# Optimization experiments

Measured on AMD Instinct MI355X. Metric: run time of the kernel, lower is better.

## Reference

```python
import jax, jax.numpy as jnp
import numpy as np

N, E = 20000, 640000
S_DIM, V_DIM, E_DIM = 128, 32 // 2, 32
EPS = 1e-8


def _vector_norm(v):
    # v: [N, V, 3] -> [N, V]
    return jnp.sqrt(jnp.clip((v * v).sum(-1), EPS))


def _gvp(s, v, W1, b1, W2, b2, Wv, Wg, bg):
    """SimpleGVP: s [N,s_in], v [N,v_in,3] -> (s_out [N,s_out], v_out [N,v_out,3]).
    Weights stored [in, out] (transpose of torch Linear)."""
    vn = _vector_norm(v)                                   # [N, v_in]
    h = jnp.concatenate([s, vn], axis=-1) @ W1 + b1        # [N, s_out]
    s_out = jax.nn.silu(h) @ W2 + b2                       # [N, s_out]
    v_proj = jnp.einsum('nvc,vw->nwc', v, Wv)              # [N, v_out, 3]
    gate = jax.nn.sigmoid(s_out @ Wg + bg)[..., None]      # [N, v_out, 1]
    return s_out, v_proj * gate


def _layer_norm(x, g, b, eps=1e-5):
    mu = x.mean(-1, keepdims=True)
    var = ((x - mu) ** 2).mean(-1, keepdims=True)
    return (x - mu) * jax.lax.rsqrt(var + eps) * g + b


def _linear_params(key, fan_in, fan_out, bias=True):
    kw, kb = jax.random.split(key)
    lim = 1.0 / np.sqrt(fan_in)
    W = jax.random.uniform(kw, (fan_in, fan_out), jnp.float32, -lim, lim)
    if bias:
        b = jax.random.uniform(kb, (fan_out,), jnp.float32, -lim, lim)
        return W, b
    return (W,)


def setup_inputs() -> dict:
    key = jax.random.key(0)
    ks = jax.random.split(key, 16)
    s = jax.random.normal(ks[0], (N, S_DIM), jnp.float32)
    v = jax.random.normal(ks[1], (N, V_DIM, 3), jnp.float32)
    edge_index = jax.random.randint(ks[2], (2, E), 0, N, jnp.int32)
    edge_s = jax.random.normal(ks[3], (E, E_DIM), jnp.float32)
    edge_v = jax.random.normal(ks[4], (E, 1, 3), jnp.float32)

    # message GVP: s_in = 2*S + E_DIM + 1 (+v_in norms), v_in = 2*V + 1
    ms_in, mv_in = 2 * S_DIM + E_DIM + 1, 2 * V_DIM + 1
    msg_W1, msg_b1 = _linear_params(ks[5], ms_in + mv_in, S_DIM)
    msg_W2, msg_b2 = _linear_params(ks[6], S_DIM, S_DIM)
    (msg_Wv,) = _linear_params(ks[7], mv_in, V_DIM, bias=False)
    msg_Wg, msg_bg = _linear_params(ks[8], S_DIM, V_DIM)

    # update GVP: s_in = 2*S, v_in = 2*V
    us_in, uv_in = 2 * S_DIM, 2 * V_DIM
    upd_W1, upd_b1 = _linear_params(ks[9], us_in + uv_in, S_DIM)
    upd_W2, upd_b2 = _linear_params(ks[10], S_DIM, S_DIM)
    (upd_Wv,) = _linear_params(ks[11], uv_in, V_DIM, bias=False)
    upd_Wg, upd_bg = _linear_params(ks[12], S_DIM, V_DIM)

    ln_g = jnp.ones((S_DIM,), jnp.float32)
    ln_b = jnp.zeros((S_DIM,), jnp.float32)

    return dict(s=s, v=v, edge_index=edge_index, edge_s=edge_s, edge_v=edge_v,
                msg_W1=msg_W1, msg_b1=msg_b1, msg_W2=msg_W2, msg_b2=msg_b2,
                msg_Wv=msg_Wv, msg_Wg=msg_Wg, msg_bg=msg_bg,
                upd_W1=upd_W1, upd_b1=upd_b1, upd_W2=upd_W2, upd_b2=upd_b2,
                upd_Wv=upd_Wv, upd_Wg=upd_Wg, upd_bg=upd_bg,
                ln_g=ln_g, ln_b=ln_b)


def reference(s, v, edge_index, edge_s, edge_v,
              msg_W1, msg_b1, msg_W2, msg_b2, msg_Wv, msg_Wg, msg_bg,
              upd_W1, upd_b1, upd_W2, upd_b2, upd_Wv, upd_Wg, upd_bg,
              ln_g, ln_b):
    src, dst = edge_index[0], edge_index[1]
    n = s.shape[0]

    # 1) per-edge message inputs (gather)
    edge_len = _vector_norm(edge_v)                                   # [E, 1]
    m_s_in = jnp.concatenate([s[src], s[dst], edge_s, edge_len], -1)  # [E, 2S+e+1]
    m_v_in = jnp.concatenate([v[src], v[dst], edge_v], 1)             # [E, 2V+1, 3]
    m_s, m_v = _gvp(m_s_in, m_v_in, msg_W1, msg_b1, msg_W2, msg_b2,
                    msg_Wv, msg_Wg, msg_bg)

    # 2) scatter-add aggregation at destination nodes
    agg_s = jax.ops.segment_sum(m_s, dst, num_segments=n)             # [N, S]
    agg_v = jax.ops.segment_sum(m_v, dst, num_segments=n)             # [N, V, 3]

    # 3) residual update
    u_s_in = jnp.concatenate([s, agg_s], -1)
    u_v_in = jnp.concatenate([v, agg_v], 1)
    ds, dv = _gvp(u_s_in, u_v_in, upd_W1, upd_b1, upd_W2, upd_b2,
                  upd_Wv, upd_Wg, upd_bg)

    s_out = _layer_norm(s + ds, ln_g, ln_b)
    v_out = v + dv
    return s_out, v_out
```

## Files before the change

kernel.cpp:

```cpp
#include <hip/hip_runtime.h>

typedef __attribute__((ext_vector_type(4))) float floatx4;
typedef __attribute__((ext_vector_type(8))) short shortx8;
typedef __attribute__((ext_vector_type(4))) short shortx4;
typedef __attribute__((ext_vector_type(4))) int intx4;
typedef __attribute__((ext_vector_type(2))) int intx2;

#define DEVI static __device__ __forceinline__

constexpr int NN = 20000;
constexpr int NE = 640000;

constexpr size_t W1ET_OFF = 0;
constexpr size_t WLEN_OFF = 8192;
constexpr size_t WCAT_OFF = 8704;
constexpr size_t W2T_OFF  = 90624;
constexpr size_t WGT_OFF  = 123392;
constexpr size_t U1T_OFF  = 127488;
constexpr size_t U2T_OFF  = 201216;
constexpr size_t UGT_OFF  = 233984;
constexpr size_t ASRC_OFF = 238080;
constexpr size_t ADST_OFF = ASRC_OFF + (size_t)NN * 128 * 2;
constexpr size_t BSRC_OFF = ADST_OFF + (size_t)NN * 128 * 2;
constexpr size_t BDST_OFF = BSRC_OFF + (size_t)NN * 64 * 2;
constexpr size_t AGG_S_OFF = BDST_OFF + (size_t)NN * 64 * 2;
constexpr size_t AGG_V_OFF = AGG_S_OFF + (size_t)NN * 128 * 2;
constexpr size_t CNT_OFF  = AGG_V_OFF + (size_t)NN * 64 * 2;
constexpr size_t OFF_OFF  = CNT_OFF + (size_t)NN * 4;
constexpr size_t PERM_OFF = OFF_OFF + (size_t)NN * 4;
constexpr size_t SD_OFF   = PERM_OFF + (size_t)NE * 4;
constexpr size_t LEV_OFF  = SD_OFF + (size_t)NE * 8;
constexpr size_t MEMSET_BYTES = (size_t)NN * 128 * 2 + (size_t)NN * 64 * 2 + (size_t)NN * 4;

DEVI float bf2f(short h) {
  union { unsigned u; float f; } c;
  c.u = ((unsigned)(unsigned short)h) << 16;
  return c.f;
}
DEVI short f2bf(float f) {
  union { float f; unsigned u; } c; c.f = f;
  unsigned x = c.u;
  return (short)((x + 0x7fffu + ((x >> 16) & 1u)) >> 16);
}
DEVI int pack2bf(float x, float y) {
  return (int)(unsigned short)f2bf(x) | ((int)(unsigned short)f2bf(y) << 16);
}
DEVI void atom_pk(short* addr, int val) {
  asm volatile("global_atomic_pk_add_bf16 %0, %1, off" : : "v"(addr), "v"(val) : "memory");
}
DEVI float sigm(float x) { return 1.0f / (1.0f + __expf(-x)); }

DEVI floatx4 mfma16(shortx8 a, shortx8 b, floatx4 c) {
  return __builtin_amdgcn_mfma_f32_16x16x32_bf16(a, b, c, 0, 0, 0);
}

__global__ void gvp_prep(const float* __restrict__ mW1, const float* __restrict__ mW2,
                         const float* __restrict__ mWg, const float* __restrict__ uW1,
                         const float* __restrict__ uW2, const float* __restrict__ uWg,
                         short* __restrict__ w1et, float* __restrict__ wlen,
                         short* __restrict__ wcat, short* __restrict__ w2t,
                         short* __restrict__ wgt, short* __restrict__ u1t,
                         short* __restrict__ u2t, short* __restrict__ ugt) {
  int i = blockIdx.x * 256 + threadIdx.x;
  if (i < 4096) { int n = i >> 5, k = i & 31; w1et[i] = f2bf(mW1[(256 + k) * 128 + n]); return; }
  i -= 4096;
  if (i < 128) { wlen[i] = mW1[288 * 128 + i] + mW1[321 * 128 + i]; return; }
  i -= 128;
  if (i < 40960) {
    int n = i / 160, k = i % 160;
    float val = 0.f;
    if (n < 128) {
      if (k < 128) val = mW1[k * 128 + n];
      else if (k < 144) val = mW1[(161 + k) * 128 + n];
    } else {
      int n2 = n - 128;
      if (k < 128) val = mW1[(128 + k) * 128 + n2];
      else if (k < 144) val = mW1[(177 + k) * 128 + n2];
    }
    wcat[i] = f2bf(val);
    return;
  }
  i -= 40960;
  if (i < 16384) { int n = i >> 7, k = i & 127; w2t[i] = f2bf(mW2[k * 128 + n]); return; }
  i -= 16384;
  if (i < 2048) { int g = i >> 7, k = i & 127; wgt[i] = f2bf(mWg[k * 16 + g]); return; }
  i -= 2048;
  if (i < 36864) { int n = i / 288, k = i % 288; u1t[i] = f2bf(uW1[k * 128 + n]); return; }
  i -= 36864;
  if (i < 16384) { int n = i >> 7, k = i & 127; u2t[i] = f2bf(uW2[k * 128 + n]); return; }
  i -= 16384;
  if (i < 2048) { int g = i >> 7, k = i & 127; ugt[i] = f2bf(uWg[k * 16 + g]); return; }
}

__global__ void gvp_hist(const int* __restrict__ eidx, int* __restrict__ cnt) {
  int e = blockIdx.x * 256 + threadIdx.x;
  if (e < NE) atomicAdd(cnt + eidx[NE + e], 1);
}

__global__ void gvp_scan(const int* __restrict__ cnt, int* __restrict__ off) {
  __shared__ int part[256];
  const int t = threadIdx.x;
  const int base = t * 79;
  int sum = 0;
  for (int j = 0; j < 79; ++j) {
    int i = base + j;
    if (i < NN) sum += cnt[i];
  }
  part[t] = sum;
  __syncthreads();
  if (t == 0) {
    int run = 0;
    for (int i = 0; i < 256; ++i) { int c = part[i]; part[i] = run; run += c; }
  }
  __syncthreads();
  int run = part[t];
  for (int j = 0; j < 79; ++j) {
    int i = base + j;
    if (i < NN) { off[i] = run; run += cnt[i]; }
  }
}

__global__ void gvp_scatter(const int* __restrict__ eidx, const float* __restrict__ ev,
                            int* __restrict__ off, int* __restrict__ perm,
                            int* __restrict__ sd, float* __restrict__ lev) {
  int e = blockIdx.x * 256 + threadIdx.x;
  if (e >= NE) return;
  int sn = eidx[e], d = eidx[NE + e];
  int pos = atomicAdd(off + d, 1);
  perm[pos] = e;
  intx2 p; p[0] = sn; p[1] = d;
  *(intx2*)(sd + (size_t)pos * 2) = p;
  const float* evp = ev + (size_t)e * 3;
  float x = evp[0], y = evp[1], z = evp[2];
  floatx4 q;
  q[0] = x; q[1] = y; q[2] = z;
  q[3] = sqrtf(fmaxf(x * x + y * y + z * z, 1e-8f));
  *(floatx4*)(lev + (size_t)pos * 4) = q;
}

__global__ __launch_bounds__(256) void gvp_nodepre(
    const float* __restrict__ s, const float* __restrict__ v,
    const short* __restrict__ wcat, const float* __restrict__ b1,
    const float* __restrict__ wv, short* __restrict__ Asrc,
    short* __restrict__ Adst, short* __restrict__ Bsrc, short* __restrict__ Bdst) {
  __shared__ __align__(16) short lx[64 * 160];
  const int tid = threadIdx.x;
  const int wid = tid >> 6;
  const int lane = tid & 63;
  const int quad = lane >> 4;
  const int l16 = lane & 15;
  const int nb0 = blockIdx.x * 64;

  intx4 z4 = {0, 0, 0, 0};
#pragma unroll
  for (int i = 0; i < 4; i++) {
    int idx = tid + i * 256;
    int r = idx >> 4, cc = (idx & 15) * 8;
    int node = nb0 + r;
    union { short sh[8]; intx4 v4; } u;
    u.v4 = z4;
    if (node < NN) {
      const float* sp = s + (size_t)node * 128 + cc;
      floatx4 f0 = *(const floatx4*)sp, f1 = *(const floatx4*)(sp + 4);
#pragma unroll
      for (int j = 0; j < 4; j++) { u.sh[j] = f2bf(f0[j]); u.sh[4 + j] = f2bf(f1[j]); }
    }
    *(intx4*)(lx + r * 160 + cc) = u.v4;
  }
  if (tid < 64) {
    int node = nb0 + tid;
    union { short sh[16]; intx4 v4[2]; } u;
#pragma unroll
    for (int j = 0; j < 16; j++) {
      float nv = 0.f;
      if (node < NN) {
        const float* vp = v + (size_t)node * 48 + j * 3;
        nv = sqrtf(fmaxf(vp[0] * vp[0] + vp[1] * vp[1] + vp[2] * vp[2], 1e-8f));
      }
      u.sh[j] = f2bf(nv);
    }
    *(intx4*)(lx + tid * 160 + 128) = u.v4[0];
    *(intx4*)(lx + tid * 160 + 136) = u.v4[1];
    *(intx4*)(lx + tid * 160 + 144) = z4;
    *(intx4*)(lx + tid * 160 + 152) = z4;
  }
  __syncthreads();

  floatx4 acc[16] = {};
#pragma unroll
  for (int kc = 0; kc < 5; kc++) {
    shortx8 a = *(const shortx8*)(lx + (wid * 16 + l16) * 160 + kc * 32 + quad * 8);
#pragma unroll
    for (int nt = 0; nt < 16; nt++) {
      shortx8 b = *(const shortx8*)(wcat + (size_t)(nt * 16 + l16) * 160 + kc * 32 + quad * 8);
      acc[nt] = mfma16(a, b, acc[nt]);
    }
  }

  float b1v[8];
#pragma unroll
  for (int nt = 0; nt < 8; nt++) b1v[nt] = b1[nt * 16 + l16];
#pragma unroll
  for (int i = 0; i < 4; i++) {
    int row = wid * 16 + quad * 4 + i;
    int node = nb0 + row;
    if (node < NN) {
      union { short sh[8]; intx4 v4; } us, ud;
#pragma unroll
      for (int nt = 0; nt < 8; nt++) {
        us.sh[nt] = f2bf(acc[nt][i] + b1v[nt]);
        ud.sh[nt] = f2bf(acc[8 + nt][i]);
      }
      *(intx4*)(Asrc + (size_t)node * 128 + l16 * 8) = us.v4;
      *(intx4*)(Adst + (size_t)node * 128 + l16 * 8) = ud.v4;
    }
  }

  {
    int node = nb0 + (tid >> 2), sub = tid & 3;
    if (node < NN) {
      float vr[48];
      const float* vp = v + (size_t)node * 48;
#pragma unroll
      for (int j = 0; j < 48; j++) vr[j] = vp[j];
      for (int w = sub * 4; w < sub * 4 + 4; w++) {
        float bs0 = 0, bs1 = 0, bs2 = 0, bd0 = 0, bd1 = 0, bd2 = 0;
#pragma unroll
        for (int j = 0; j < 16; j++) {
          float w0 = wv[j * 16 + w], w1 = wv[(16 + j) * 16 + w];
          bs0 += vr[j * 3 + 0] * w0; bs1 += vr[j * 3 + 1] * w0; bs2 += vr[j * 3 + 2] * w0;
          bd0 += vr[j * 3 + 0] * w1; bd1 += vr[j * 3 + 1] * w1; bd2 += vr[j * 3 + 2] * w1;
        }
        union { short sh[4]; intx2 v2; } ub, ud2;
        ub.sh[0] = f2bf(bs0); ub.sh[1] = f2bf(bs1); ub.sh[2] = f2bf(bs2); ub.sh[3] = 0;
        ud2.sh[0] = f2bf(bd0); ud2.sh[1] = f2bf(bd1); ud2.sh[2] = f2bf(bd2); ud2.sh[3] = 0;
        *(intx2*)(Bsrc + (size_t)node * 64 + w * 4) = ub.v2;
        *(intx2*)(Bdst + (size_t)node * 64 + w * 4) = ud2.v2;
      }
    }
  }
}

__global__ __launch_bounds__(256, 5) void gvp_edge(
    const int* __restrict__ perm, const int* __restrict__ sd,
    const float* __restrict__ lev, const float* __restrict__ es,
    const short* __restrict__ w1et, const float* __restrict__ wlen,
    const short* __restrict__ w2t, const short* __restrict__ wgt,
    const short* __restrict__ Asrc, const short* __restrict__ Adst,
    const short* __restrict__ Bsrc, const short* __restrict__ Bdst,
    const float* __restrict__ b2, const float* __restrict__ wv,
    const float* __restrict__ bg, short* __restrict__ agg_s,
    short* __restrict__ agg_v) {
  __shared__ __align__(16) short lh_all[4 * 16 * 136];
  __shared__ __align__(16) float lv_all[4 * 16 * 50];
  __shared__ int lsrc[64];
  __shared__ int ldst[64];
  __shared__ float lev4[64][4];

  const int tid = threadIdx.x;
  const int wid = tid >> 6;
  const int lane = tid & 63;
  const int quad = lane >> 4;
  const int l16 = lane & 15;
  const int e0 = blockIdx.x * 64;

  if (tid < 64) {
    intx2 p = *(const intx2*)(sd + (size_t)(e0 + tid) * 2);
    lsrc[tid] = p[0];
    ldst[tid] = p[1];
  } else if (tid < 128) {
    int er = tid - 64;
    floatx4 q = *(const floatx4*)(lev + (size_t)(e0 + er) * 4);
    lev4[er][0] = q[0]; lev4[er][1] = q[1]; lev4[er][2] = q[2]; lev4[er][3] = q[3];
  }
  __syncthreads();

  short* lh = lh_all + wid * 2176;
  float* lv = lv_all + wid * 800;

  const int erow = wid * 16 + l16;
  const int pe = perm[e0 + erow];
  const float* ep = es + (size_t)pe * 32 + quad * 8;
  floatx4 ea = *(const floatx4*)ep;
  floatx4 eb = *(const floatx4*)(ep + 4);
  shortx8 afrag;
#pragma unroll
  for (int j = 0; j < 4; j++) { afrag[j] = f2bf(ea[j]); afrag[4 + j] = f2bf(eb[j]); }
  floatx4 acc[8];
#pragma unroll
  for (int nt = 0; nt < 8; nt++) {
    shortx8 b = *(const shortx8*)(w1et + (nt * 16 + l16) * 32 + quad * 8);
    floatx4 z = {0.f, 0.f, 0.f, 0.f};
    acc[nt] = mfma16(afrag, b, z);
  }

  int srcn[4], dstn[4];
  float lenr[4];
#pragma unroll
  for (int i = 0; i < 4; i++) {
    int r = wid * 16 + quad * 4 + i;
    srcn[i] = lsrc[r]; dstn[i] = ldst[r]; lenr[i] = lev4[r][3];
  }

#pragma unroll
  for (int i = 0; i < 4; i++) {
    shortx8 s8 = *(const shortx8*)(Asrc + (size_t)srcn[i] * 128 + l16 * 8);
    shortx8 d8 = *(const shortx8*)(Adst + (size_t)dstn[i] * 128 + l16 * 8);
#pragma unroll
    for (int nt = 0; nt < 8; nt++) acc[nt][i] += bf2f(s8[nt]) + bf2f(d8[nt]);
  }
#pragma unroll
  for (int nt = 0; nt < 8; nt++) {
    float wl = wlen[nt * 16 + l16];
#pragma unroll
    for (int i = 0; i < 4; i++) acc[nt][i] += lenr[i] * wl;
  }

#pragma unroll
  for (int nt = 0; nt < 8; nt++)
#pragma unroll
    for (int i = 0; i < 4; i++) {
      float h = acc[nt][i];
      lh[(quad * 4 + i) * 136 + nt * 16 + l16] = f2bf(h * sigm(h));
    }

  floatx4 acc2[8] = {};
#pragma unroll
  for (int kc = 0; kc < 4; kc++) {
    shortx8 a = *(const shortx8*)(lh + l16 * 136 + kc * 32 + quad * 8);
#pragma unroll
    for (int nt = 0; nt < 8; nt++) {
      shortx8 b = *(const shortx8*)(w2t + (size_t)(nt * 16 + l16) * 128 + kc * 32 + quad * 8);
      acc2[nt] = mfma16(a, b, acc2[nt]);
    }
  }

#pragma unroll
  for (int nt = 0; nt < 8; nt++) {
    float b2v = b2[nt * 16 + l16];
#pragma unroll
    for (int i = 0; i < 4; i++)
      lh[(quad * 4 + i) * 136 + nt * 16 + l16] = f2bf(acc2[nt][i] + b2v);
  }

  floatx4 acc3 = {0.f, 0.f, 0.f, 0.f};
#pragma unroll
  for (int kc = 0; kc < 4; kc++) {
    shortx8 a = *(const shortx8*)(lh + l16 * 136 + kc * 32 + quad * 8);
    shortx8 b = *(const shortx8*)(wgt + l16 * 128 + kc * 32 + quad * 8);
    acc3 = mfma16(a, b, acc3);
  }

  float wv32v = wv[32 * 16 + l16];
  float bgv = bg[l16];
#pragma unroll
  for (int i = 0; i < 4; i++) {
    int r = wid * 16 + quad * 4 + i;
    shortx4 bs = *(const shortx4*)(Bsrc + (size_t)srcn[i] * 64 + l16 * 4);
    shortx4 bd = *(const shortx4*)(Bdst + (size_t)dstn[i] * 64 + l16 * 4);
    float vx = bf2f(bs[0]) + bf2f(bd[0]) + lev4[r][0] * wv32v;
    float vy = bf2f(bs[1]) + bf2f(bd[1]) + lev4[r][1] * wv32v;
    float vz = bf2f(bs[2]) + bf2f(bd[2]) + lev4[r][2] * wv32v;
    float g = sigm(acc3[i] + bgv);
    float* dp = lv + (quad * 4 + i) * 50 + l16 * 3;
    dp[0] = g * vx; dp[1] = g * vy; dp[2] = g * vz;
  }

  const int rbase = wid * 16;
  int r = 0;
  while (r < 16) {
    int d = ldst[rbase + r];
    int r2 = r + 1;
    while (r2 < 16 && ldst[rbase + r2] == d) ++r2;
    float s0 = 0.f, s1 = 0.f;
    for (int row = r; row < r2; ++row) {
      int pv = *(const int*)(lh + row * 136 + 2 * lane);
      s0 += bf2f((short)(pv & 0xffff));
      s1 += bf2f((short)((unsigned)pv >> 16));
    }
    atom_pk(agg_s + (size_t)d * 128 + 2 * lane, pack2bf(s0, s1));
    if (lane < 32) {
      int w = lane >> 1;
      float a0 = 0.f, a1 = 0.f;
      if ((lane & 1) == 0) {
        for (int row = r; row < r2; ++row) {
          a0 += lv[row * 50 + w * 3];
          a1 += lv[row * 50 + w * 3 + 1];
        }
      } else {
        for (int row = r; row < r2; ++row) a0 += lv[row * 50 + w * 3 + 2];
      }
      atom_pk(agg_v + (size_t)d * 64 + 2 * lane, pack2bf(a0, a1));
    }
    r = r2;
  }
}

__global__ __launch_bounds__(256) void gvp_node(
    const float* __restrict__ s, const float* __restrict__ v,
    const short* __restrict__ agg_s, const short* __restrict__ agg_v,
    const short* __restrict__ u1t, const short* __restrict__ u2t,
    const short* __restrict__ ugt, const float* __restrict__ b1,
    const float* __restrict__ b2, const float* __restrict__ uwv,
    const float* __restrict__ bg, const float* __restrict__ lng,
    const float* __restrict__ lnb, float* __restrict__ out_s,
    float* __restrict__ out_v) {
  __shared__ __align__(16) short lx[64 * 352];
  const int tid = threadIdx.x;
  const int wid = tid >> 6;
  const int lane = tid & 63;
  const int quad = lane >> 4;
  const int l16 = lane & 15;
  const int nb0 = blockIdx.x * 64;

  intx4 z4 = {0, 0, 0, 0};
#pragma unroll
  for (int i = 0; i < 4; i++) {
    int idx = tid + i * 256;
    int r = idx >> 4, cc = (idx & 15) * 8;
    int node = nb0 + r;
    union { short sh[8]; intx4 v4; } u;
    u.v4 = z4;
    if (node < NN) {
      const float* sp = s + (size_t)node * 128 + cc;
      floatx4 f0 = *(const floatx4*)sp, f1 = *(const floatx4*)(sp + 4);
#pragma unroll
      for (int j = 0; j < 4; j++) { u.sh[j] = f2bf(f0[j]); u.sh[4 + j] = f2bf(f1[j]); }
    }
    *(intx4*)(lx + r * 288 + cc) = u.v4;
  }
#pragma unroll
  for (int i = 0; i < 4; i++) {
    int idx = tid + i * 256;
    int r = idx >> 4, cc = (idx & 15) * 8;
    int node = nb0 + r;
    intx4 val = z4;
    if (node < NN) val = *(const intx4*)(agg_s + (size_t)node * 128 + cc);
    *(intx4*)(lx + r * 288 + 128 + cc) = val;
  }
  {
    int r = tid >> 2, p = tid & 3;
    int node = nb0 + r;
    int w0 = (p & 1) * 8;
    if (p < 2) {
#pragma unroll
      for (int w = 0; w < 8; w++) {
        float nv = 0.f;
        if (node < NN) {
          const float* vp = v + (size_t)node * 48 + (w0 + w) * 3;
          nv = sqrtf(fmaxf(vp[0] * vp[0] + vp[1] * vp[1] + vp[2] * vp[2], 1e-8f));
        }
        lx[r * 288 + 256 + w0 + w] = f2bf(nv);
      }
    } else {
#pragma unroll
      for (int w = 0; w < 8; w++) {
        float nv = 0.f;
        if (node < NN) {
          const short* ap = agg_v + (size_t)node * 64 + (w0 + w) * 4;
          float x = bf2f(ap[0]), y = bf2f(ap[1]), zz = bf2f(ap[2]);
          nv = sqrtf(fmaxf(x * x + y * y + zz * zz, 1e-8f));
        }
        lx[r * 288 + 272 + w0 + w] = f2bf(nv);
      }
    }
  }
  __syncthreads();

  floatx4 acc[8] = {};
#pragma unroll
  for (int kc = 0; kc < 9; kc++) {
    shortx8 a = *(const shortx8*)(lx + (wid * 16 + l16) * 288 + kc * 32 + quad * 8);
#pragma unroll
    for (int nt = 0; nt < 8; nt++) {
      shortx8 b = *(const shortx8*)(u1t + (size_t)(nt * 16 + l16) * 288 + kc * 32 + quad * 8);
      acc[nt] = mfma16(a, b, acc[nt]);
    }
  }
  __syncthreads();

  short* lh = lx;
#pragma unroll
  for (int nt = 0; nt < 8; nt++)
#pragma unroll
    for (int i = 0; i < 4; i++) {
      int row = wid * 16 + quad * 4 + i;
      float h = acc[nt][i] + b1[nt * 16 + l16];
      lh[row * 136 + nt * 16 + l16] = f2bf(h * sigm(h));
    }

  floatx4 acc2[8] = {};
#pragma unroll
  for (int kc = 0; kc < 4; kc++) {
    shortx8 a = *(const shortx8*)(lh + (wid * 16 + l16) * 136 + kc * 32 + quad * 8);
#pragma unroll
    for (int nt = 0; nt < 8; nt++) {
      shortx8 b = *(const shortx8*)(u2t + (size_t)(nt * 16 + l16) * 128 + kc * 32 + quad * 8);
      acc2[nt] = mfma16(a, b, acc2[nt]);
    }
  }

#pragma unroll
  for (int nt = 0; nt < 8; nt++)
#pragma unroll
    for (int i = 0; i < 4; i++) {
      int row = wid * 16 + quad * 4 + i;
      int col = nt * 16 + l16;
      int node = nb0 + row;
      float ds = acc2[nt][i] + b2[col];
      lh[row * 136 + col] = f2bf(ds);
      float sv = (node < NN) ? s[(size_t)node * 128 + col] : 0.f;
      acc2[nt][i] = sv + ds;
    }

#pragma unroll
  for (int i = 0; i < 4; i++) {
    float sum = 0.f, sq = 0.f;
#pragma unroll
    for (int nt = 0; nt < 8; nt++) { float t = acc2[nt][i]; sum += t; sq += t * t; }
    for (int off = 1; off < 16; off <<= 1) {
      sum += __shfl_xor(sum, off);
      sq += __shfl_xor(sq, off);
    }
    float mean = sum * (1.f / 128.f);
    float var = sq * (1.f / 128.f) - mean * mean;
    float inv = rsqrtf(fmaxf(var, 0.f) + 1e-5f);
    int node = nb0 + wid * 16 + quad * 4 + i;
    if (node < NN) {
#pragma unroll
      for (int nt = 0; nt < 8; nt++) {
        int col = nt * 16 + l16;
        float o = (acc2[nt][i] - mean) * inv * lng[col] + lnb[col];
        out_s[(size_t)node * 128 + col] = o;
      }
    }
  }

  float* lmvf = (float*)((char*)lx + 17408) + wid * 1600;
  {
    int e = lane >> 2, p = lane & 3;
    int node = nb0 + wid * 16 + e;
    if (p < 2) {
      floatx4* dp = (floatx4*)(lmvf + e * 100 + p * 24);
      if (node < NN) {
        const floatx4* sp = (const floatx4*)(v + (size_t)node * 48 + p * 24);
#pragma unroll
        for (int j = 0; j < 6; j++) dp[j] = sp[j];
      } else {
        floatx4 zf = {0.f, 0.f, 0.f, 0.f};
#pragma unroll
        for (int j = 0; j < 6; j++) dp[j] = zf;
      }
    } else {
      int wbase = (p - 2) * 8;
#pragma unroll
      for (int w = 0; w < 8; w++) {
        float x = 0.f, y = 0.f, zz = 0.f;
        if (node < NN) {
          const short* ap = agg_v + (size_t)node * 64 + (wbase + w) * 4;
          x = bf2f(ap[0]); y = bf2f(ap[1]); zz = bf2f(ap[2]);
        }
        float* dp = lmvf + e * 100 + 48 + (wbase + w) * 3;
        dp[0] = x; dp[1] = y; dp[2] = zz;
      }
    }
  }

  floatx4 acc3 = {0.f, 0.f, 0.f, 0.f};
#pragma unroll
  for (int kc = 0; kc < 4; kc++) {
    shortx8 a = *(const shortx8*)(lh + (wid * 16 + l16) * 136 + kc * 32 + quad * 8);
    shortx8 b = *(const shortx8*)(ugt + l16 * 128 + kc * 32 + quad * 8);
    acc3 = mfma16(a, b, acc3);
  }

  float vm[4][3] = {};
  for (int j = 0; j < 32; j++) {
    float wj = uwv[j * 16 + l16];
#pragma unroll
    for (int i = 0; i < 4; i++) {
      int e = quad * 4 + i;
      vm[i][0] += wj * lmvf[e * 100 + j * 3 + 0];
      vm[i][1] += wj * lmvf[e * 100 + j * 3 + 1];
      vm[i][2] += wj * lmvf[e * 100 + j * 3 + 2];
    }
  }
#pragma unroll
  for (int i = 0; i < 4; i++) {
    int node = nb0 + wid * 16 + quad * 4 + i;
    if (node < NN) {
      float g = sigm(acc3[i] + bg[l16]);
      size_t base = (size_t)node * 48 + l16 * 3;
      out_v[base + 0] = v[base + 0] + g * vm[i][0];
      out_v[base + 1] = v[base + 1] + g * vm[i][1];
      out_v[base + 2] = v[base + 2] + g * vm[i][2];
    }
  }
}

extern "C" void kernel_launch(void* const* d_in, const int* in_sizes, int n_in,
                              void* d_out, int out_size, void* d_ws, size_t ws_size,
                              hipStream_t stream) {
  const float* s = (const float*)d_in[0];
  const float* v = (const float*)d_in[1];
  const int* eidx = (const int*)d_in[2];
  const float* es = (const float*)d_in[3];
  const float* ev = (const float*)d_in[4];
  const float* mW1 = (const float*)d_in[5];
  const float* mb1 = (const float*)d_in[6];
  const float* mW2 = (const float*)d_in[7];
  const float* mb2 = (const float*)d_in[8];
  const float* mWv = (const float*)d_in[9];
  const float* mWg = (const float*)d_in[10];
  const float* mbg = (const float*)d_in[11];
  const float* uW1 = (const float*)d_in[12];
  const float* ub1 = (const float*)d_in[13];
  const float* uW2 = (const float*)d_in[14];
  const float* ub2 = (const float*)d_in[15];
  const float* uWv = (const float*)d_in[16];
  const float* uWg = (const float*)d_in[17];
  const float* ubg = (const float*)d_in[18];
  const float* lng = (const float*)d_in[19];
  const float* lnb = (const float*)d_in[20];

  char* ws = (char*)d_ws;
  short* w1et = (short*)(ws + W1ET_OFF);
  float* wlen = (float*)(ws + WLEN_OFF);
  short* wcat = (short*)(ws + WCAT_OFF);
  short* w2t = (short*)(ws + W2T_OFF);
  short* wgt = (short*)(ws + WGT_OFF);
  short* u1t = (short*)(ws + U1T_OFF);
  short* u2t = (short*)(ws + U2T_OFF);
  short* ugt = (short*)(ws + UGT_OFF);
  short* Asrc = (short*)(ws + ASRC_OFF);
  short* Adst = (short*)(ws + ADST_OFF);
  short* Bsrc = (short*)(ws + BSRC_OFF);
  short* Bdst = (short*)(ws + BDST_OFF);
  short* agg_s = (short*)(ws + AGG_S_OFF);
  short* agg_v = (short*)(ws + AGG_V_OFF);
  int* cnt = (int*)(ws + CNT_OFF);
  int* off = (int*)(ws + OFF_OFF);
  int* perm = (int*)(ws + PERM_OFF);
  int* sd = (int*)(ws + SD_OFF);
  float* lev = (float*)(ws + LEV_OFF);

  hipMemsetAsync(ws + AGG_S_OFF, 0, MEMSET_BYTES, stream);
  gvp_prep<<<465, 256, 0, stream>>>(mW1, mW2, mWg, uW1, uW2, uWg,
                                    w1et, wlen, wcat, w2t, wgt, u1t, u2t, ugt);
  gvp_hist<<<NE / 256, 256, 0, stream>>>(eidx, cnt);
  gvp_scan<<<1, 256, 0, stream>>>(cnt, off);
  gvp_scatter<<<NE / 256, 256, 0, stream>>>(eidx, ev, off, perm, sd, lev);
  gvp_nodepre<<<(NN + 63) / 64, 256, 0, stream>>>(s, v, wcat, mb1, mWv,
                                                  Asrc, Adst, Bsrc, Bdst);
  gvp_edge<<<NE / 64, 256, 0, stream>>>(perm, sd, lev, es, w1et, wlen, w2t, wgt,
                                        Asrc, Adst, Bsrc, Bdst, mb2, mWv, mbg,
                                        agg_s, agg_v);
  gvp_node<<<(NN + 63) / 64, 256, 0, stream>>>(s, v, agg_s, agg_v, u1t, u2t, ugt,
                                               ub1, ub2, uWv, ubg, lng, lnb,
                                               (float*)d_out,
                                               (float*)d_out + (size_t)NN * 128);
}
```

Measured before the change: 627.4 us.

## Fold message W2 into gate and update weights, aggregating pre-W2 activations

```diff
diff --git a/kernel.cpp b/kernel.cpp
--- a/kernel.cpp
+++ b/kernel.cpp
@@ -14,12 +14,13 @@
 constexpr size_t W1ET_OFF = 0;
 constexpr size_t WLEN_OFF = 8192;
 constexpr size_t WCAT_OFF = 8704;
-constexpr size_t W2T_OFF  = 90624;
-constexpr size_t WGT_OFF  = 123392;
-constexpr size_t U1T_OFF  = 127488;
-constexpr size_t U2T_OFF  = 201216;
-constexpr size_t UGT_OFF  = 233984;
-constexpr size_t ASRC_OFF = 238080;
+constexpr size_t W2GT_OFF = 90624;
+constexpr size_t CG_OFF   = 94720;
+constexpr size_t U1T_OFF  = 94784;
+constexpr size_t B2U_OFF  = 168512;
+constexpr size_t U2T_OFF  = 169024;
+constexpr size_t UGT_OFF  = 201792;
+constexpr size_t ASRC_OFF = 205888;
 constexpr size_t ADST_OFF = ASRC_OFF + (size_t)NN * 128 * 2;
 constexpr size_t BSRC_OFF = ADST_OFF + (size_t)NN * 128 * 2;
 constexpr size_t BDST_OFF = BSRC_OFF + (size_t)NN * 64 * 2;
@@ -28,8 +29,6 @@
 constexpr size_t CNT_OFF  = AGG_V_OFF + (size_t)NN * 64 * 2;
 constexpr size_t OFF_OFF  = CNT_OFF + (size_t)NN * 4;
 constexpr size_t PERM_OFF = OFF_OFF + (size_t)NN * 4;
-constexpr size_t SD_OFF   = PERM_OFF + (size_t)NE * 4;
-constexpr size_t LEV_OFF  = SD_OFF + (size_t)NE * 8;
 constexpr size_t MEMSET_BYTES = (size_t)NN * 128 * 2 + (size_t)NN * 64 * 2 + (size_t)NN * 4;
 
 DEVI float bf2f(short h) {
@@ -48,19 +47,21 @@
 DEVI void atom_pk(short* addr, int val) {
   asm volatile("global_atomic_pk_add_bf16 %0, %1, off" : : "v"(addr), "v"(val) : "memory");
 }
-DEVI float sigm(float x) { return 1.0f / (1.0f + __expf(-x)); }
+DEVI float sigm(float x) { return __builtin_amdgcn_rcpf(1.0f + __expf(-x)); }
 
 DEVI floatx4 mfma16(shortx8 a, shortx8 b, floatx4 c) {
   return __builtin_amdgcn_mfma_f32_16x16x32_bf16(a, b, c, 0, 0, 0);
 }
 
 __global__ void gvp_prep(const float* __restrict__ mW1, const float* __restrict__ mW2,
-                         const float* __restrict__ mWg, const float* __restrict__ uW1,
+                         const float* __restrict__ mWg, const float* __restrict__ mb2,
+                         const float* __restrict__ mbg, const float* __restrict__ uW1,
                          const float* __restrict__ uW2, const float* __restrict__ uWg,
                          short* __restrict__ w1et, float* __restrict__ wlen,
-                         short* __restrict__ wcat, short* __restrict__ w2t,
-                         short* __restrict__ wgt, short* __restrict__ u1t,
-                         short* __restrict__ u2t, short* __restrict__ ugt) {
+                         short* __restrict__ wcat, short* __restrict__ w2gt,
+                         float* __restrict__ cg, short* __restrict__ u1t,
+                         float* __restrict__ b2u, short* __restrict__ u2t,
+                         short* __restrict__ ugt) {
   int i = blockIdx.x * 256 + threadIdx.x;
   if (i < 4096) { int n = i >> 5, k = i & 31; w1et[i] = f2bf(mW1[(256 + k) * 128 + n]); return; }
   i -= 4096;
@@ -81,12 +82,53 @@
     return;
   }
   i -= 40960;
-  if (i < 16384) { int n = i >> 7, k = i & 127; w2t[i] = f2bf(mW2[k * 128 + n]); return; }
-  i -= 16384;
-  if (i < 2048) { int g = i >> 7, k = i & 127; wgt[i] = f2bf(mWg[k * 16 + g]); return; }
+  if (i < 2048) {
+    int g = i >> 7, k = i & 127;
+    float acc = 0.f;
+#pragma unroll 4
+    for (int c4 = 0; c4 < 32; ++c4) {
+      floatx4 wr = *(const floatx4*)(mW2 + k * 128 + c4 * 4);
+      acc += wr[0] * mWg[(c4 * 4 + 0) * 16 + g] + wr[1] * mWg[(c4 * 4 + 1) * 16 + g] +
+             wr[2] * mWg[(c4 * 4 + 2) * 16 + g] + wr[3] * mWg[(c4 * 4 + 3) * 16 + g];
+    }
+    w2gt[i] = f2bf(acc);
+    return;
+  }
   i -= 2048;
-  if (i < 36864) { int n = i / 288, k = i % 288; u1t[i] = f2bf(uW1[k * 128 + n]); return; }
+  if (i < 16) {
+    float acc = mbg[i];
+    for (int c = 0; c < 128; ++c) acc += mb2[c] * mWg[c * 16 + i];
+    cg[i] = acc;
+    return;
+  }
+  i -= 16;
+  if (i < 36864) {
+    int n = i / 288, k = i % 288;
+    if (k < 128 || k >= 256) {
+      u1t[i] = f2bf(uW1[k * 128 + n]);
+    } else {
+      int j = k - 128;
+      float acc = 0.f;
+#pragma unroll 4
+      for (int c4 = 0; c4 < 32; ++c4) {
+        floatx4 wr = *(const floatx4*)(mW2 + j * 128 + c4 * 4);
+        acc += wr[0] * uW1[(128 + c4 * 4 + 0) * 128 + n] +
+               wr[1] * uW1[(128 + c4 * 4 + 1) * 128 + n] +
+               wr[2] * uW1[(128 + c4 * 4 + 2) * 128 + n] +
+               wr[3] * uW1[(128 + c4 * 4 + 3) * 128 + n];
+      }
+      u1t[i] = f2bf(acc);
+    }
+    return;
+  }
   i -= 36864;
+  if (i < 128) {
+    float acc = 0.f;
+    for (int c = 0; c < 128; ++c) acc += mb2[c] * uW1[(128 + c) * 128 + i];
+    b2u[i] = acc;
+    return;
+  }
+  i -= 128;
   if (i < 16384) { int n = i >> 7, k = i & 127; u2t[i] = f2bf(uW2[k * 128 + n]); return; }
   i -= 16384;
   if (i < 2048) { int g = i >> 7, k = i & 127; ugt[i] = f2bf(uWg[k * 16 + g]); return; }
@@ -120,22 +162,13 @@
   }
 }
 
-__global__ void gvp_scatter(const int* __restrict__ eidx, const float* __restrict__ ev,
-                            int* __restrict__ off, int* __restrict__ perm,
-                            int* __restrict__ sd, float* __restrict__ lev) {
+__global__ void gvp_scatter(const int* __restrict__ eidx, int* __restrict__ off,
+                            int* __restrict__ perm) {
   int e = blockIdx.x * 256 + threadIdx.x;
   if (e >= NE) return;
-  int sn = eidx[e], d = eidx[NE + e];
+  int d = eidx[NE + e];
   int pos = atomicAdd(off + d, 1);
   perm[pos] = e;
-  intx2 p; p[0] = sn; p[1] = d;
-  *(intx2*)(sd + (size_t)pos * 2) = p;
-  const float* evp = ev + (size_t)e * 3;
-  float x = evp[0], y = evp[1], z = evp[2];
-  floatx4 q;
-  q[0] = x; q[1] = y; q[2] = z;
-  q[3] = sqrtf(fmaxf(x * x + y * y + z * z, 1e-8f));
-  *(floatx4*)(lev + (size_t)pos * 4) = q;
 }
 
 __global__ __launch_bounds__(256) void gvp_nodepre(
@@ -241,18 +274,17 @@
   }
 }
 
-__global__ __launch_bounds__(256, 5) void gvp_edge(
-    const int* __restrict__ perm, const int* __restrict__ sd,
-    const float* __restrict__ lev, const float* __restrict__ es,
+__global__ __launch_bounds__(256, 8) void gvp_edge(
+    const int* __restrict__ perm, const int* __restrict__ eidx,
+    const float* __restrict__ ev, const float* __restrict__ es,
     const short* __restrict__ w1et, const float* __restrict__ wlen,
-    const short* __restrict__ w2t, const short* __restrict__ wgt,
-    const short* __restrict__ Asrc, const short* __restrict__ Adst,
-    const short* __restrict__ Bsrc, const short* __restrict__ Bdst,
-    const float* __restrict__ b2, const float* __restrict__ wv,
-    const float* __restrict__ bg, short* __restrict__ agg_s,
+    const short* __restrict__ w2gt, const short* __restrict__ Asrc,
+    const short* __restrict__ Adst, const short* __restrict__ Bsrc,
+    const short* __restrict__ Bdst, const float* __restrict__ cg,
+    const float* __restrict__ wv, short* __restrict__ agg_s,
     short* __restrict__ agg_v) {
   __shared__ __align__(16) short lh_all[4 * 16 * 136];
-  __shared__ __align__(16) float lv_all[4 * 16 * 50];
+  __shared__ int lpe[64];
   __shared__ int lsrc[64];
   __shared__ int ldst[64];
   __shared__ float lev4[64][4];
@@ -265,21 +297,24 @@
   const int e0 = blockIdx.x * 64;
 
   if (tid < 64) {
-    intx2 p = *(const intx2*)(sd + (size_t)(e0 + tid) * 2);
-    lsrc[tid] = p[0];
-    ldst[tid] = p[1];
+    int pe = perm[e0 + tid];
+    lpe[tid] = pe;
+    lsrc[tid] = eidx[pe];
+    ldst[tid] = eidx[NE + pe];
   } else if (tid < 128) {
     int er = tid - 64;
-    floatx4 q = *(const floatx4*)(lev + (size_t)(e0 + er) * 4);
-    lev4[er][0] = q[0]; lev4[er][1] = q[1]; lev4[er][2] = q[2]; lev4[er][3] = q[3];
+    int pe = perm[e0 + er];
+    const float* evp = ev + (size_t)pe * 3;
+    float x = evp[0], y = evp[1], z = evp[2];
+    lev4[er][0] = x; lev4[er][1] = y; lev4[er][2] = z;
+    lev4[er][3] = sqrtf(fmaxf(x * x + y * y + z * z, 1e-8f));
   }
   __syncthreads();
 
   short* lh = lh_all + wid * 2176;
-  float* lv = lv_all + wid * 800;
 
   const int erow = wid * 16 + l16;
-  const int pe = perm[e0 + erow];
+  const int pe = lpe[erow];
   const float* ep = es + (size_t)pe * 32 + quad * 8;
   floatx4 ea = *(const floatx4*)ep;
   floatx4 eb = *(const floatx4*)(ep + 4);
@@ -324,35 +359,17 @@
       lh[(quad * 4 + i) * 136 + nt * 16 + l16] = f2bf(h * sigm(h));
     }
 
-  floatx4 acc2[8] = {};
+  floatx4 acc3 = {0.f, 0.f, 0.f, 0.f};
 #pragma unroll
   for (int kc = 0; kc < 4; kc++) {
     shortx8 a = *(const shortx8*)(lh + l16 * 136 + kc * 32 + quad * 8);
-#pragma unroll
-    for (int nt = 0; nt < 8; nt++) {
-      shortx8 b = *(const shortx8*)(w2t + (size_t)(nt * 16 + l16) * 128 + kc * 32 + quad * 8);
-      acc2[nt] = mfma16(a, b, acc2[nt]);
-    }
-  }
-
-#pragma unroll
-  for (int nt = 0; nt < 8; nt++) {
-    float b2v = b2[nt * 16 + l16];
-#pragma unroll
-    for (int i = 0; i < 4; i++)
-      lh[(quad * 4 + i) * 136 + nt * 16 + l16] = f2bf(acc2[nt][i] + b2v);
-  }
-
-  floatx4 acc3 = {0.f, 0.f, 0.f, 0.f};
-#pragma unroll
-  for (int kc = 0; kc < 4; kc++) {
-    shortx8 a = *(const shortx8*)(lh + l16 * 136 + kc * 32 + quad * 8);
-    shortx8 b = *(const shortx8*)(wgt + l16 * 128 + kc * 32 + quad * 8);
+    shortx8 b = *(const shortx8*)(w2gt + l16 * 128 + kc * 32 + quad * 8);
     acc3 = mfma16(a, b, acc3);
   }
 
   float wv32v = wv[32 * 16 + l16];
-  float bgv = bg[l16];
+  float cgv = cg[l16];
+  float gv[4][3];
 #pragma unroll
   for (int i = 0; i < 4; i++) {
     int r = wid * 16 + quad * 4 + i;
@@ -361,9 +378,8 @@
     float vx = bf2f(bs[0]) + bf2f(bd[0]) + lev4[r][0] * wv32v;
     float vy = bf2f(bs[1]) + bf2f(bd[1]) + lev4[r][1] * wv32v;
     float vz = bf2f(bs[2]) + bf2f(bd[2]) + lev4[r][2] * wv32v;
-    float g = sigm(acc3[i] + bgv);
-    float* dp = lv + (quad * 4 + i) * 50 + l16 * 3;
-    dp[0] = g * vx; dp[1] = g * vy; dp[2] = g * vz;
+    float g = sigm(acc3[i] + cgv);
+    gv[i][0] = g * vx; gv[i][1] = g * vy; gv[i][2] = g * vz;
   }
 
   const int rbase = wid * 16;
@@ -379,18 +395,18 @@
       s1 += bf2f((short)((unsigned)pv >> 16));
     }
     atom_pk(agg_s + (size_t)d * 128 + 2 * lane, pack2bf(s0, s1));
-    if (lane < 32) {
-      int w = lane >> 1;
-      float a0 = 0.f, a1 = 0.f;
-      if ((lane & 1) == 0) {
-        for (int row = r; row < r2; ++row) {
-          a0 += lv[row * 50 + w * 3];
-          a1 += lv[row * 50 + w * 3 + 1];
-        }
-      } else {
-        for (int row = r; row < r2; ++row) a0 += lv[row * 50 + w * 3 + 2];
-      }
-      atom_pk(agg_v + (size_t)d * 64 + 2 * lane, pack2bf(a0, a1));
+    float vx = 0.f, vy = 0.f, vz = 0.f;
+#pragma unroll
+    for (int i = 0; i < 4; ++i) {
+      int row = quad * 4 + i;
+      if (row >= r && row < r2) { vx += gv[i][0]; vy += gv[i][1]; vz += gv[i][2]; }
+    }
+    vx += __shfl_xor(vx, 16); vy += __shfl_xor(vy, 16); vz += __shfl_xor(vz, 16);
+    vx += __shfl_xor(vx, 32); vy += __shfl_xor(vy, 32); vz += __shfl_xor(vz, 32);
+    if (quad == 0) {
+      short* ap = agg_v + (size_t)d * 64 + l16 * 4;
+      atom_pk(ap, pack2bf(vx, vy));
+      atom_pk(ap + 2, pack2bf(vz, 0.f));
     }
     r = r2;
   }
@@ -399,6 +415,7 @@
 __global__ __launch_bounds__(256) void gvp_node(
     const float* __restrict__ s, const float* __restrict__ v,
     const short* __restrict__ agg_s, const short* __restrict__ agg_v,
+    const int* __restrict__ cnt, const float* __restrict__ b2u,
     const short* __restrict__ u1t, const short* __restrict__ u2t,
     const short* __restrict__ ugt, const float* __restrict__ b1,
     const float* __restrict__ b2, const float* __restrict__ uwv,
@@ -413,6 +430,13 @@
   const int l16 = lane & 15;
   const int nb0 = blockIdx.x * 64;
 
+  float cntf[4];
+#pragma unroll
+  for (int i = 0; i < 4; i++) {
+    int node = nb0 + wid * 16 + quad * 4 + i;
+    cntf[i] = (node < NN) ? (float)cnt[node] : 0.f;
+  }
+
   intx4 z4 = {0, 0, 0, 0};
 #pragma unroll
   for (int i = 0; i < 4; i++) {
@@ -485,8 +509,9 @@
 #pragma unroll
     for (int i = 0; i < 4; i++) {
       int row = wid * 16 + quad * 4 + i;
-      float h = acc[nt][i] + b1[nt * 16 + l16];
-      lh[row * 136 + nt * 16 + l16] = f2bf(h * sigm(h));
+      int col = nt * 16 + l16;
+      float h = acc[nt][i] + b1[col] + cntf[i] * b2u[col];
+      lh[row * 136 + col] = f2bf(h * sigm(h));
     }
 
   floatx4 acc2[8] = {};
@@ -627,9 +652,10 @@
   short* w1et = (short*)(ws + W1ET_OFF);
   float* wlen = (float*)(ws + WLEN_OFF);
   short* wcat = (short*)(ws + WCAT_OFF);
-  short* w2t = (short*)(ws + W2T_OFF);
-  short* wgt = (short*)(ws + WGT_OFF);
+  short* w2gt = (short*)(ws + W2GT_OFF);
+  float* cg = (float*)(ws + CG_OFF);
   short* u1t = (short*)(ws + U1T_OFF);
+  float* b2u = (float*)(ws + B2U_OFF);
   short* u2t = (short*)(ws + U2T_OFF);
   short* ugt = (short*)(ws + UGT_OFF);
   short* Asrc = (short*)(ws + ASRC_OFF);
@@ -641,22 +667,20 @@
   int* cnt = (int*)(ws + CNT_OFF);
   int* off = (int*)(ws + OFF_OFF);
   int* perm = (int*)(ws + PERM_OFF);
-  int* sd = (int*)(ws + SD_OFF);
-  float* lev = (float*)(ws + LEV_OFF);
 
   hipMemsetAsync(ws + AGG_S_OFF, 0, MEMSET_BYTES, stream);
-  gvp_prep<<<465, 256, 0, stream>>>(mW1, mW2, mWg, uW1, uW2, uWg,
-                                    w1et, wlen, wcat, w2t, wgt, u1t, u2t, ugt);
+  gvp_prep<<<402, 256, 0, stream>>>(mW1, mW2, mWg, mb2, mbg, uW1, uW2, uWg,
+                                    w1et, wlen, wcat, w2gt, cg, u1t, b2u, u2t, ugt);
   gvp_hist<<<NE / 256, 256, 0, stream>>>(eidx, cnt);
   gvp_scan<<<1, 256, 0, stream>>>(cnt, off);
-  gvp_scatter<<<NE / 256, 256, 0, stream>>>(eidx, ev, off, perm, sd, lev);
+  gvp_scatter<<<NE / 256, 256, 0, stream>>>(eidx, off, perm);
   gvp_nodepre<<<(NN + 63) / 64, 256, 0, stream>>>(s, v, wcat, mb1, mWv,
                                                   Asrc, Adst, Bsrc, Bdst);
-  gvp_edge<<<NE / 64, 256, 0, stream>>>(perm, sd, lev, es, w1et, wlen, w2t, wgt,
-                                        Asrc, Adst, Bsrc, Bdst, mb2, mWv, mbg,
+  gvp_edge<<<NE / 64, 256, 0, stream>>>(perm, eidx, ev, es, w1et, wlen, w2gt,
+                                        Asrc, Adst, Bsrc, Bdst, cg, mWv,
                                         agg_s, agg_v);
-  gvp_node<<<(NN + 63) / 64, 256, 0, stream>>>(s, v, agg_s, agg_v, u1t, u2t, ugt,
-                                               ub1, ub2, uWv, ubg, lng, lnb,
-                                               (float*)d_out,
+  gvp_node<<<(NN + 63) / 64, 256, 0, stream>>>(s, v, agg_s, agg_v, cnt, b2u,
+                                               u1t, u2t, ugt, ub1, ub2, uWv, ubg,
+                                               lng, lnb, (float*)d_out,
                                                (float*)d_out + (size_t)NN * 128);
 }
```

Measured after the change: 579.3 us. -7.7%, faster.
